# Kernel tuning notes

Hardware: AMD Instinct MI355X
Metric: run time of the kernel (lower is better)

Reference implementation:

```python
import jax, jax.numpy as jnp
import numpy as np

C = 384
NUM_HEADS = 6
HEAD_SIZE = C // NUM_HEADS
EPS = 1e-5


def setup_inputs() -> dict:
    key = jax.random.key(0)
    ks = jax.random.split(key, 16)
    sc = lambda *s: 0.02
    inp = {
        'x': jax.random.normal(ks[0], (256, 256, C), dtype=jnp.float32),
        'Wq': jax.random.normal(ks[1], (NUM_HEADS, C, HEAD_SIZE), dtype=jnp.float32) * 0.02,
        'Wk': jax.random.normal(ks[2], (NUM_HEADS, C, HEAD_SIZE), dtype=jnp.float32) * 0.02,
        'Wv': jax.random.normal(ks[3], (NUM_HEADS, C, HEAD_SIZE), dtype=jnp.float32) * 0.02,
        'Wp': jax.random.normal(ks[4], (C, C), dtype=jnp.float32) * 0.02,
        'bp': jnp.zeros((C,), dtype=jnp.float32),
        'W1': jax.random.normal(ks[5], (C, 4 * C), dtype=jnp.float32) * 0.02,
        'b1': jnp.zeros((4 * C,), dtype=jnp.float32),
        'W2': jax.random.normal(ks[6], (4 * C, C), dtype=jnp.float32) * 0.02,
        'b2': jnp.zeros((C,), dtype=jnp.float32),
        'g1': jnp.ones((C,), dtype=jnp.float32),
        'be1': jnp.zeros((C,), dtype=jnp.float32),
        'g2': jnp.ones((C,), dtype=jnp.float32),
        'be2': jnp.zeros((C,), dtype=jnp.float32),
    }
    return inp


def _layernorm(x, g, b):
    mu = jnp.mean(x, axis=-1, keepdims=True)
    var = jnp.mean(jnp.square(x - mu), axis=-1, keepdims=True)
    return (x - mu) * jax.lax.rsqrt(var + EPS) * g + b


def reference(x, Wq, Wk, Wv, Wp, bp, W1, b1, W2, b2, g1, be1, g2, be2):
    B, T, _ = x.shape
    # --- attention sublayer (dropout = identity in eval) ---
    h = _layernorm(x, g1, be1)
    Q = jnp.einsum('btc,hcd->bhtd', h, Wq)
    K = jnp.einsum('btc,hcd->bhtd', h, Wk)
    V = jnp.einsum('btc,hcd->bhtd', h, Wv)
    scores = jnp.einsum('bhtd,bhsd->bhts', Q, K) / jnp.sqrt(jnp.float32(HEAD_SIZE))
    causal = jnp.tril(jnp.ones((T, T), dtype=bool))
    scores = jnp.where(causal, scores, -jnp.inf)
    attn = jax.nn.softmax(scores, axis=-1)
    out = jnp.einsum('bhts,bhsd->bhtd', attn, V)  # [B,H,T,d]
    out = out.transpose(0, 2, 1, 3).reshape(B, T, C)  # concat heads
    x = x + out @ Wp + bp
    # --- feed-forward sublayer ---
    h2 = _layernorm(x, g2, be2)
    ff = jax.nn.relu(h2 @ W1 + b1) @ W2 + b2
    return x + ff
```

## Files before the change

### kernel.cpp

```cpp
#include <hip/hip_runtime.h>
#include <hip/hip_bf16.h>


typedef __attribute__((ext_vector_type(8))) short bf16x8;
typedef __attribute__((ext_vector_type(4))) float f32x4;
typedef unsigned short u16;
typedef unsigned int u32;

#define MFMA16(a, b, c) __builtin_amdgcn_mfma_f32_16x16x32_bf16((a), (b), (c), 0, 0, 0)

__device__ __forceinline__ void gl2lds16(const void* g, void* l) {
  __builtin_amdgcn_global_load_lds((const __attribute__((address_space(1))) u32*)g,
                                   (__attribute__((address_space(3))) u32*)l, 16, 0, 0);
}

__device__ __forceinline__ u16 f2bf(float f) {
  __hip_bfloat16 h = __float2bfloat16(f);
  return *(u16*)&h;
}
__device__ __forceinline__ float bf2f(u16 u) {
  __hip_bfloat16 h;
  *(u16*)&h = u;
  return __bfloat162float(h);
}
__device__ __forceinline__ u32 pack2(float lo, float hi) {
  return (u32)f2bf(lo) | ((u32)f2bf(hi) << 16);
}

template <int HAS_BIAS, int HAS_RES, int RELU, int OUT_MODE>
__global__ __launch_bounds__(256) void gemm_bt(const u16* __restrict__ A,
                                               const u16* __restrict__ Bt,
                                               const float* __restrict__ bias,
                                               const float* res, void* outp,
                                               int M, int N, int K, int gx) {
  __shared__ __attribute__((aligned(16))) u16 As[128 * 64];
  __shared__ __attribute__((aligned(16))) u16 Bs[128 * 64];
  const int bid = blockIdx.x;
  const int s = bid >> 3, xcd = bid & 7;
  const int gy8 = gridDim.x / (8 * gx);
  const int nI = s % gx, mC = s / gx;
  const int m0 = (xcd * gy8 + mC) * 128, n0 = nI * 128;
  const int w = threadIdx.x >> 6, l = threadIdx.x & 63;
  const int lm = l & 15, quad = l >> 4;
  const int wm = (w >> 1) * 64, wn = (w & 1) * 64;
  f32x4 acc[4][4];
#pragma unroll
  for (int i = 0; i < 4; ++i)
#pragma unroll
    for (int j = 0; j < 4; ++j) acc[i][j] = 0.f;

  for (int k0 = 0; k0 < K; k0 += 64) {
#pragma unroll
    for (int j = 0; j < 4; ++j) {
      int ell = (w * 4 + j) * 64 + l;
      int row = ell >> 3;
      int cs = ell & 7;
      int cg = cs ^ (row & 7);
      gl2lds16(A + (size_t)(m0 + row) * K + k0 + cg * 8, &As[(w * 4 + j) * 64 * 8]);
      gl2lds16(Bt + (size_t)(n0 + row) * K + k0 + cg * 8, &Bs[(w * 4 + j) * 64 * 8]);
    }
    __syncthreads();
#pragma unroll
    for (int ks = 0; ks < 2; ++ks) {
      bf16x8 af[4], bfb[4];
#pragma unroll
      for (int i = 0; i < 4; ++i) {
        int r = wm + i * 16 + lm;
        af[i] = *(const bf16x8*)&As[r * 64 + (((ks * 4 + quad) ^ (r & 7)) * 8)];
      }
#pragma unroll
      for (int j = 0; j < 4; ++j) {
        int r = wn + j * 16 + lm;
        bfb[j] = *(const bf16x8*)&Bs[r * 64 + (((ks * 4 + quad) ^ (r & 7)) * 8)];
      }
#pragma unroll
      for (int i = 0; i < 4; ++i)
#pragma unroll
        for (int j = 0; j < 4; ++j) acc[i][j] = MFMA16(af[i], bfb[j], acc[i][j]);
    }
    __syncthreads();
  }
#pragma unroll
  for (int i = 0; i < 4; ++i) {
#pragma unroll
    for (int j = 0; j < 4; ++j) {
      int col = n0 + wn + j * 16 + lm;
      float bs = HAS_BIAS ? bias[col] : 0.f;
#pragma unroll
      for (int r = 0; r < 4; ++r) {
        int row = m0 + wm + i * 16 + quad * 4 + r;
        float v = acc[i][j][r] + bs;
        if (RELU) v = fmaxf(v, 0.f);
        if (HAS_RES) v += res[(size_t)row * N + col];
        if (OUT_MODE == 0) {
          ((float*)outp)[(size_t)row * N + col] = v;
        } else if (OUT_MODE == 1) {
          ((u16*)outp)[(size_t)row * N + col] = f2bf(v);
        } else {
          int sel = col / 384;
          int rem = col - sel * 384;
          int hh = rem >> 6, dd = rem & 63;
          ((u16*)outp)[((size_t)(sel * 6 + hh) * 65536 + row) * 64 + dd] = f2bf(v);
        }
      }
    }
  }
}

__global__ __launch_bounds__(256) void ln_kernel(const float* __restrict__ x,
                                                 const float* __restrict__ g,
                                                 const float* __restrict__ be,
                                                 u16* __restrict__ out) {
  int row = blockIdx.x * 4 + (threadIdx.x >> 6);
  int l = threadIdx.x & 63;
  const float2* xr = (const float2*)(x + (size_t)row * 384 + l * 6);
  float2 t0 = xr[0], t1 = xr[1], t2 = xr[2];
  float v[6] = {t0.x, t0.y, t1.x, t1.y, t2.x, t2.y};
  float s = 0.f;
#pragma unroll
  for (int i = 0; i < 6; ++i) s += v[i];
#pragma unroll
  for (int o = 1; o < 64; o <<= 1) s += __shfl_xor(s, o, 64);
  float mu = s * (1.f / 384.f);
  float var = 0.f;
#pragma unroll
  for (int i = 0; i < 6; ++i) {
    float d = v[i] - mu;
    var += d * d;
  }
#pragma unroll
  for (int o = 1; o < 64; o <<= 1) var += __shfl_xor(var, o, 64);
  float rs = rsqrtf(var * (1.f / 384.f) + 1e-5f);
  const float2* gg = (const float2*)(g + l * 6);
  const float2* bb = (const float2*)(be + l * 6);
  float2 g0 = gg[0], g1 = gg[1], g2 = gg[2];
  float2 b0 = bb[0], b1 = bb[1], b2 = bb[2];
  float gv[6] = {g0.x, g0.y, g1.x, g1.y, g2.x, g2.y};
  float bv[6] = {b0.x, b0.y, b1.x, b1.y, b2.x, b2.y};
  float o_[6];
#pragma unroll
  for (int i = 0; i < 6; ++i) o_[i] = (v[i] - mu) * rs * gv[i] + bv[i];
  u32* orow = (u32*)(out + (size_t)row * 384 + l * 6);
  orow[0] = pack2(o_[0], o_[1]);
  orow[1] = pack2(o_[2], o_[3]);
  orow[2] = pack2(o_[4], o_[5]);
}

__global__ void wT_kernel(const float* __restrict__ in, u16* __restrict__ out,
                          int K, int N) {
  int idx = blockIdx.x * 256 + threadIdx.x;
  if (idx >= K * N) return;
  int n = idx / K, k = idx - n * K;
  out[idx] = f2bf(in[(size_t)k * N + n]);
}

__global__ void qkvT_kernel(const float* __restrict__ W, u16* __restrict__ out) {
  int idx = blockIdx.x * 256 + threadIdx.x;
  if (idx >= 6 * 384 * 64) return;
  int r = idx / 384;
  int c = idx - r * 384;
  int h = r >> 6, d = r & 63;
  out[idx] = f2bf(W[(size_t)(h * 384 + c) * 64 + d]);
}

template <int TQ>
__device__ __forceinline__ void attn_body(const u16* __restrict__ qkv,
                                          u16* __restrict__ attnout,
                                          unsigned char* smx) {
  constexpr int NFULL = (TQ + 1) * 64;
  constexpr int NJ = NFULL / 16;
  constexpr int KSTEPS = NFULL / 32;
  int bh = blockIdx.y;
  int h = bh % 6, b = bh / 6;
  int tid = threadIdx.x;
  int w = tid >> 6, l = tid & 63;
  int lm = l & 15, quad = l >> 4;

  u16* Qs = (u16*)smx;
  u16* Ks = (u16*)(smx + 9216);
  u16* P = (u16*)smx;
  u16* Vt = (u16*)(smx + 32768);

  const u16* Qg = qkv + ((size_t)h * 65536 + b * 256 + TQ * 64) * 64;
  const u16* Kg = qkv + ((size_t)(6 + h) * 65536 + b * 256) * 64;
  const u16* Vg = qkv + ((size_t)(12 + h) * 65536 + b * 256) * 64;

  for (int i = tid; i < 64 * 8; i += 256) {
    int r = i >> 3, cs = i & 7;
    *(bf16x8*)&Qs[r * 72 + cs * 8] = *(const bf16x8*)&Qg[r * 64 + cs * 8];
  }
  for (int i = tid; i < NFULL * 8; i += 256) {
    int r = i >> 3, cs = i & 7;
    *(bf16x8*)&Ks[r * 72 + cs * 8] = *(const bf16x8*)&Kg[r * 64 + cs * 8];
  }
  __syncthreads();

  f32x4 sacc[NJ];
#pragma unroll
  for (int jt = 0; jt < NJ; ++jt) sacc[jt] = 0.f;
#pragma unroll
  for (int kk = 0; kk < 2; ++kk) {
    bf16x8 aq = *(const bf16x8*)&Qs[(w * 16 + lm) * 72 + kk * 32 + quad * 8];
#pragma unroll
    for (int jt = 0; jt < NJ; ++jt) {
      bf16x8 bk = *(const bf16x8*)&Ks[(jt * 16 + lm) * 72 + kk * 32 + quad * 8];
      sacc[jt] = MFMA16(aq, bk, sacc[jt]);
    }
  }
  __syncthreads();

  int trow = TQ * 64 + w * 16 + quad * 4;
  float inv_l[4];
#pragma unroll
  for (int reg = 0; reg < 4; ++reg) {
    float m_ = -3.0e38f;
#pragma unroll
    for (int jt = 0; jt < NJ; ++jt) {
      int col = jt * 16 + lm;
      if (col <= trow + reg) m_ = fmaxf(m_, sacc[jt][reg]);
    }
#pragma unroll
    for (int o = 1; o < 16; o <<= 1) m_ = fmaxf(m_, __shfl_xor(m_, o, 16));
    float s_ = 0.f;
#pragma unroll
    for (int jt = 0; jt < NJ; ++jt) {
      int col = jt * 16 + lm;
      float p = (col <= trow + reg) ? __expf(0.125f * (sacc[jt][reg] - m_)) : 0.f;
      sacc[jt][reg] = p;
      s_ += p;
    }
#pragma unroll
    for (int o = 1; o < 16; o <<= 1) s_ += __shfl_xor(s_, o, 16);
    inv_l[reg] = 1.f / s_;
  }
#pragma unroll
  for (int jt = 0; jt < NJ; ++jt) {
#pragma unroll
    for (int reg = 0; reg < 4; ++reg) {
      int m = w * 16 + quad * 4 + reg;
      int col = jt * 16 + lm;
      P[m * 256 + (col ^ ((m & 7) * 8))] = f2bf(sacc[jt][reg] * inv_l[reg]);
    }
  }
  for (int i = tid; i < NFULL * 8; i += 256) {
    int sr = i >> 3, cs = i & 7;
    bf16x8 vv = *(const bf16x8*)&Vg[sr * 64 + cs * 8];
#pragma unroll
    for (int j = 0; j < 8; ++j) {
      int d = cs * 8 + j;
      Vt[d * 256 + (sr ^ ((d & 7) * 8))] = (u16)vv[j];
    }
  }
  __syncthreads();

  f32x4 oacc[4];
#pragma unroll
  for (int jt = 0; jt < 4; ++jt) oacc[jt] = 0.f;
#pragma unroll
  for (int ks = 0; ks < KSTEPS; ++ks) {
    int m = w * 16 + lm;
    int kc = ks * 32 + quad * 8;
    bf16x8 ap = *(const bf16x8*)&P[m * 256 + (kc ^ ((m & 7) * 8))];
#pragma unroll
    for (int jt = 0; jt < 4; ++jt) {
      int n = jt * 16 + lm;
      bf16x8 bv = *(const bf16x8*)&Vt[n * 256 + (kc ^ ((n & 7) * 8))];
      oacc[jt] = MFMA16(ap, bv, oacc[jt]);
    }
  }
  u16* Og = attnout + ((size_t)(b * 256 + TQ * 64)) * 384 + h * 64;
#pragma unroll
  for (int jt = 0; jt < 4; ++jt)
#pragma unroll
    for (int r = 0; r < 4; ++r)
      Og[(size_t)(w * 16 + quad * 4 + r) * 384 + jt * 16 + lm] = f2bf(oacc[jt][r]);
}

__global__ __launch_bounds__(256) void attn_all(const u16* __restrict__ qkv,
                                                u16* __restrict__ attnout) {
  __shared__ __attribute__((aligned(16))) unsigned char smx[65536];
  switch (blockIdx.x) {
    case 0: attn_body<0>(qkv, attnout, smx); break;
    case 1: attn_body<1>(qkv, attnout, smx); break;
    case 2: attn_body<2>(qkv, attnout, smx); break;
    default: attn_body<3>(qkv, attnout, smx); break;
  }
}

extern "C" void kernel_launch(void* const* d_in, const int* in_sizes, int n_in,
                              void* d_out, int out_size, void* d_ws, size_t ws_size,
                              hipStream_t stream) {
  const float* x = (const float*)d_in[0];
  const float* Wq = (const float*)d_in[1];
  const float* Wk = (const float*)d_in[2];
  const float* Wv = (const float*)d_in[3];
  const float* Wp = (const float*)d_in[4];
  const float* bp = (const float*)d_in[5];
  const float* W1 = (const float*)d_in[6];
  const float* b1 = (const float*)d_in[7];
  const float* W2 = (const float*)d_in[8];
  const float* b2 = (const float*)d_in[9];
  const float* g1 = (const float*)d_in[10];
  const float* be1 = (const float*)d_in[11];
  const float* g2 = (const float*)d_in[12];
  const float* be2 = (const float*)d_in[13];
  float* out = (float*)d_out;

  const int BT = 65536;
  char* ws = (char*)d_ws;
  u16* qkv = (u16*)(ws);
  u16* attnout = (u16*)(ws + 150994944);
  u16* ff1 = (u16*)(ws);
  u16* h = (u16*)(ws + 201326592);
  u16* WqkvT = (u16*)(ws + 251658240);
  u16* WpT = (u16*)(ws + 252542976);
  u16* W1T = (u16*)(ws + 252837888);
  u16* W2T = (u16*)(ws + 254017536);

  qkvT_kernel<<<576, 256, 0, stream>>>(Wq, WqkvT);
  qkvT_kernel<<<576, 256, 0, stream>>>(Wk, WqkvT + 384 * 384);
  qkvT_kernel<<<576, 256, 0, stream>>>(Wv, WqkvT + 2 * 384 * 384);
  wT_kernel<<<576, 256, 0, stream>>>(Wp, WpT, 384, 384);
  wT_kernel<<<2304, 256, 0, stream>>>(W1, W1T, 384, 1536);
  wT_kernel<<<2304, 256, 0, stream>>>(W2, W2T, 1536, 384);

  ln_kernel<<<BT / 4, 256, 0, stream>>>(x, g1, be1, h);
  gemm_bt<0, 0, 0, 2><<<9 * 512, 256, 0, stream>>>(h, WqkvT, nullptr, nullptr,
                                                   qkv, BT, 1152, 384, 9);
  attn_all<<<dim3(4, 1536), 256, 0, stream>>>(qkv, attnout);
  gemm_bt<1, 1, 0, 0><<<3 * 512, 256, 0, stream>>>(attnout, WpT, bp, x, out,
                                                   BT, 384, 384, 3);
  ln_kernel<<<BT / 4, 256, 0, stream>>>(out, g2, be2, h);
  gemm_bt<1, 0, 1, 1><<<12 * 512, 256, 0, stream>>>(h, W1T, b1, nullptr, ff1,
                                                    BT, 1536, 384, 12);
  gemm_bt<1, 1, 0, 0><<<3 * 512, 256, 0, stream>>>(ff1, W2T, b2, out, out,
                                                   BT, 384, 1536, 3);
}
```

Baseline: 811.2 us.

## Double-buffer GEMM LDS tiles with K=32 steps and tile weight transposes

The GEMM main loop now uses two LDS buffers of 128x32 tiles with a new swizzle, and issues the global-to-LDS loads for the next K step before running the MFMAs on the current one. This removes one barrier per step and overlaps the loads with compute. The cost is a shorter K step, so a barrier now comes every 32 elements instead of 64. The weight transpose kernels also switch to shared-memory 32x32 tiles, so both their reads and writes are coalesced.

```diff
diff --git a/kernel.cpp b/kernel.cpp
--- a/kernel.cpp
+++ b/kernel.cpp
@@ -25,6 +25,10 @@
 }
 __device__ __forceinline__ u32 pack2(float lo, float hi) {
   return (u32)f2bf(lo) | ((u32)f2bf(hi) << 16);
+}
+
+__device__ __forceinline__ int sw_slot(int r, int c) {
+  return (r >> 1) * 8 + ((((r & 1) << 2) | c) ^ ((r >> 1) & 7));
 }
 
 template <int HAS_BIAS, int HAS_RES, int RELU, int OUT_MODE>
@@ -33,8 +37,8 @@
                                                const float* __restrict__ bias,
                                                const float* res, void* outp,
                                                int M, int N, int K, int gx) {
-  __shared__ __attribute__((aligned(16))) u16 As[128 * 64];
-  __shared__ __attribute__((aligned(16))) u16 Bs[128 * 64];
+  __shared__ __attribute__((aligned(16))) u16 As[2][4096];
+  __shared__ __attribute__((aligned(16))) u16 Bs[2][4096];
   const int bid = blockIdx.x;
   const int s = bid >> 3, xcd = bid & 7;
   const int gy8 = gridDim.x / (8 * gx);
@@ -43,43 +47,61 @@
   const int w = threadIdx.x >> 6, l = threadIdx.x & 63;
   const int lm = l & 15, quad = l >> 4;
   const int wm = (w >> 1) * 64, wn = (w & 1) * 64;
+
+  const int st0 = threadIdx.x, st1 = threadIdx.x + 256;
+  int R2, p, ar0, ac0, ar1, ac1;
+  R2 = st0 >> 3; p = (st0 & 7) ^ (R2 & 7); ar0 = 2 * R2 + (p >> 2); ac0 = p & 3;
+  R2 = st1 >> 3; p = (st1 & 7) ^ (R2 & 7); ar1 = 2 * R2 + (p >> 2); ac1 = p & 3;
+  const u16* Ag0 = A + (size_t)(m0 + ar0) * K + ac0 * 8;
+  const u16* Ag1 = A + (size_t)(m0 + ar1) * K + ac1 * 8;
+  const u16* Bg0 = Bt + (size_t)(n0 + ar0) * K + ac0 * 8;
+  const u16* Bg1 = Bt + (size_t)(n0 + ar1) * K + ac1 * 8;
+  u16* La0 = &As[0][(w * 64) * 8];
+  u16* La1 = &As[0][(256 + w * 64) * 8];
+  u16* Lb0 = &Bs[0][(w * 64) * 8];
+  u16* Lb1 = &Bs[0][(256 + w * 64) * 8];
+
+  int afo[4], bfo[4];
+#pragma unroll
+  for (int i = 0; i < 4; ++i) afo[i] = sw_slot(wm + i * 16 + lm, quad) * 8;
+#pragma unroll
+  for (int j = 0; j < 4; ++j) bfo[j] = sw_slot(wn + j * 16 + lm, quad) * 8;
+
   f32x4 acc[4][4];
 #pragma unroll
   for (int i = 0; i < 4; ++i)
 #pragma unroll
     for (int j = 0; j < 4; ++j) acc[i][j] = 0.f;
 
-  for (int k0 = 0; k0 < K; k0 += 64) {
-#pragma unroll
-    for (int j = 0; j < 4; ++j) {
-      int ell = (w * 4 + j) * 64 + l;
-      int row = ell >> 3;
-      int cs = ell & 7;
-      int cg = cs ^ (row & 7);
-      gl2lds16(A + (size_t)(m0 + row) * K + k0 + cg * 8, &As[(w * 4 + j) * 64 * 8]);
-      gl2lds16(Bt + (size_t)(n0 + row) * K + k0 + cg * 8, &Bs[(w * 4 + j) * 64 * 8]);
-    }
+  const int nk = K >> 5;
+  gl2lds16(Ag0, La0);
+  gl2lds16(Ag1, La1);
+  gl2lds16(Bg0, Lb0);
+  gl2lds16(Bg1, Lb1);
+  __syncthreads();
+
+  for (int k = 0; k < nk; ++k) {
+    const int cb = k & 1;
+    if (k + 1 < nk) {
+      const int nb = cb ^ 1;
+      const int go = (k + 1) * 32;
+      gl2lds16(Ag0 + go, La0 + nb * 4096);
+      gl2lds16(Ag1 + go, La1 + nb * 4096);
+      gl2lds16(Bg0 + go, Lb0 + nb * 4096);
+      gl2lds16(Bg1 + go, Lb1 + nb * 4096);
+    }
+    bf16x8 af[4], bfb[4];
+#pragma unroll
+    for (int i = 0; i < 4; ++i) af[i] = *(const bf16x8*)&As[cb][afo[i]];
+#pragma unroll
+    for (int j = 0; j < 4; ++j) bfb[j] = *(const bf16x8*)&Bs[cb][bfo[j]];
+#pragma unroll
+    for (int i = 0; i < 4; ++i)
+#pragma unroll
+      for (int j = 0; j < 4; ++j) acc[i][j] = MFMA16(af[i], bfb[j], acc[i][j]);
     __syncthreads();
-#pragma unroll
-    for (int ks = 0; ks < 2; ++ks) {
-      bf16x8 af[4], bfb[4];
-#pragma unroll
-      for (int i = 0; i < 4; ++i) {
-        int r = wm + i * 16 + lm;
-        af[i] = *(const bf16x8*)&As[r * 64 + (((ks * 4 + quad) ^ (r & 7)) * 8)];
-      }
-#pragma unroll
-      for (int j = 0; j < 4; ++j) {
-        int r = wn + j * 16 + lm;
-        bfb[j] = *(const bf16x8*)&Bs[r * 64 + (((ks * 4 + quad) ^ (r & 7)) * 8)];
-      }
-#pragma unroll
-      for (int i = 0; i < 4; ++i)
-#pragma unroll
-        for (int j = 0; j < 4; ++j) acc[i][j] = MFMA16(af[i], bfb[j], acc[i][j]);
-    }
-    __syncthreads();
-  }
+  }
+
 #pragma unroll
   for (int i = 0; i < 4; ++i) {
 #pragma unroll
@@ -146,21 +168,36 @@
   orow[2] = pack2(o_[4], o_[5]);
 }
 
-__global__ void wT_kernel(const float* __restrict__ in, u16* __restrict__ out,
-                          int K, int N) {
-  int idx = blockIdx.x * 256 + threadIdx.x;
-  if (idx >= K * N) return;
-  int n = idx / K, k = idx - n * K;
-  out[idx] = f2bf(in[(size_t)k * N + n]);
-}
-
-__global__ void qkvT_kernel(const float* __restrict__ W, u16* __restrict__ out) {
-  int idx = blockIdx.x * 256 + threadIdx.x;
-  if (idx >= 6 * 384 * 64) return;
-  int r = idx / 384;
-  int c = idx - r * 384;
-  int h = r >> 6, d = r & 63;
-  out[idx] = f2bf(W[(size_t)(h * 384 + c) * 64 + d]);
+__global__ __launch_bounds__(256) void wT_kernel(const float* __restrict__ in,
+                                                 u16* __restrict__ out, int K,
+                                                 int N) {
+  __shared__ float tile[32][33];
+  int n0 = blockIdx.x * 32, k0 = blockIdx.y * 32;
+  int tx = threadIdx.x & 31, ty = threadIdx.x >> 5;
+#pragma unroll
+  for (int i = 0; i < 4; ++i)
+    tile[ty + i * 8][tx] = in[(size_t)(k0 + ty + i * 8) * N + n0 + tx];
+  __syncthreads();
+#pragma unroll
+  for (int i = 0; i < 4; ++i)
+    out[(size_t)(n0 + ty + i * 8) * K + k0 + tx] = f2bf(tile[tx][ty + i * 8]);
+}
+
+__global__ __launch_bounds__(256) void qkvT_kernel(const float* __restrict__ W,
+                                                   u16* __restrict__ out) {
+  __shared__ float tile[32][33];
+  int h = blockIdx.z;
+  const float* in = W + (size_t)h * 384 * 64;
+  u16* o = out + (size_t)h * 64 * 384;
+  int n0 = blockIdx.x * 32, k0 = blockIdx.y * 32;
+  int tx = threadIdx.x & 31, ty = threadIdx.x >> 5;
+#pragma unroll
+  for (int i = 0; i < 4; ++i)
+    tile[ty + i * 8][tx] = in[(size_t)(k0 + ty + i * 8) * 64 + n0 + tx];
+  __syncthreads();
+#pragma unroll
+  for (int i = 0; i < 4; ++i)
+    o[(size_t)(n0 + ty + i * 8) * 384 + k0 + tx] = f2bf(tile[tx][ty + i * 8]);
 }
 
 template <int TQ>
@@ -225,9 +262,9 @@
 #pragma unroll
     for (int jt = 0; jt < NJ; ++jt) {
       int col = jt * 16 + lm;
-      float p = (col <= trow + reg) ? __expf(0.125f * (sacc[jt][reg] - m_)) : 0.f;
-      sacc[jt][reg] = p;
-      s_ += p;
+      float pv = (col <= trow + reg) ? __expf(0.125f * (sacc[jt][reg] - m_)) : 0.f;
+      sacc[jt][reg] = pv;
+      s_ += pv;
     }
 #pragma unroll
     for (int o = 1; o < 16; o <<= 1) s_ += __shfl_xor(s_, o, 16);
@@ -317,12 +354,12 @@
   u16* W1T = (u16*)(ws + 252837888);
   u16* W2T = (u16*)(ws + 254017536);
 
-  qkvT_kernel<<<576, 256, 0, stream>>>(Wq, WqkvT);
-  qkvT_kernel<<<576, 256, 0, stream>>>(Wk, WqkvT + 384 * 384);
-  qkvT_kernel<<<576, 256, 0, stream>>>(Wv, WqkvT + 2 * 384 * 384);
-  wT_kernel<<<576, 256, 0, stream>>>(Wp, WpT, 384, 384);
-  wT_kernel<<<2304, 256, 0, stream>>>(W1, W1T, 384, 1536);
-  wT_kernel<<<2304, 256, 0, stream>>>(W2, W2T, 1536, 384);
+  qkvT_kernel<<<dim3(2, 12, 6), 256, 0, stream>>>(Wq, WqkvT);
+  qkvT_kernel<<<dim3(2, 12, 6), 256, 0, stream>>>(Wk, WqkvT + 384 * 384);
+  qkvT_kernel<<<dim3(2, 12, 6), 256, 0, stream>>>(Wv, WqkvT + 2 * 384 * 384);
+  wT_kernel<<<dim3(12, 12), 256, 0, stream>>>(Wp, WpT, 384, 384);
+  wT_kernel<<<dim3(48, 12), 256, 0, stream>>>(W1, W1T, 384, 1536);
+  wT_kernel<<<dim3(12, 48), 256, 0, stream>>>(W2, W2T, 1536, 384);
 
   ln_kernel<<<BT / 4, 256, 0, stream>>>(x, g1, be1, h);
   gemm_bt<0, 0, 0, 2><<<9 * 512, 256, 0, stream>>>(h, WqkvT, nullptr, nullptr,
```

Result: slower. 846.8 us (+4.4%).
